# Kernel tuning notes

Hardware: AMD Instinct MI355X
Metric: run time of the kernel (lower is better)

The kernel has to match this reference:

```python
import jax, jax.numpy as jnp
import numpy as np

N = 20000      # nodes
E = 320000     # edges (avg degree 16)
IN, HID, OUT, H = 128, 32, 32, 8
NEG_SLOPE = 0.2


def _gat_conv(x, src, dst, W, al, ar, b):
    """One DGL-style GATConv. x: [N, F_in], W: [F_in, H*D], al/ar: [H, D], b: [H*D].
    Returns [N, H, D]."""
    n = x.shape[0]
    Hh, D = al.shape
    feat = (x @ W).reshape(n, Hh, D)                      # [N,H,D]
    el = jnp.sum(feat * al[None], axis=-1)                # [N,H]
    er = jnp.sum(feat * ar[None], axis=-1)                # [N,H]
    e = jax.nn.leaky_relu(el[src] + er[dst], NEG_SLOPE)   # [E,H]
    # edge softmax over incoming edges of each dst node (stable)
    emax = jax.ops.segment_max(e, dst, num_segments=n)    # [N,H]
    ee = jnp.exp(e - emax[dst])                           # [E,H]
    denom = jax.ops.segment_sum(ee, dst, num_segments=n)  # [N,H]
    alpha = ee / denom[dst]                               # [E,H]
    msg = feat[src] * alpha[:, :, None]                   # [E,H,D] gather+weight
    out = jax.ops.segment_sum(msg, dst, num_segments=n)   # [N,H,D] scatter-add
    return out + b.reshape(1, Hh, D)


def setup_inputs() -> dict:
    key = jax.random.key(0)
    ks = jax.random.split(key, 11)
    return {
        "x":   jax.random.normal(ks[0], (N, IN), dtype=jnp.float32),
        "src": jax.random.randint(ks[1], (E,), 0, N, dtype=jnp.int32),
        "dst": jax.random.randint(ks[2], (E,), 0, N, dtype=jnp.int32),
        "W1":  jax.random.normal(ks[3], (IN, H * HID), dtype=jnp.float32) * 0.1,
        "al1": jax.random.normal(ks[4], (H, HID), dtype=jnp.float32) * 0.1,
        "ar1": jax.random.normal(ks[5], (H, HID), dtype=jnp.float32) * 0.1,
        "b1":  jnp.zeros((H * HID,), dtype=jnp.float32),
        "W2":  jax.random.normal(ks[6], (HID, H * OUT), dtype=jnp.float32) * 0.1,
        "al2": jax.random.normal(ks[7], (H, OUT), dtype=jnp.float32) * 0.1,
        "ar2": jax.random.normal(ks[8], (H, OUT), dtype=jnp.float32) * 0.1,
        "b2":  jnp.zeros((H * OUT,), dtype=jnp.float32),
    }


def reference(x, src, dst, W1, al1, ar1, b1, W2, al2, ar2, b2):
    h = _gat_conv(x, src, dst, W1, al1, ar1, b1)          # [N,H,HID]
    h = jnp.mean(jax.nn.relu(h), axis=1)                  # [N,HID]
    h = _gat_conv(h, src, dst, W2, al2, ar2, b2)          # [N,H,OUT]
    return jnp.mean(h, axis=1)                            # [N,OUT]
```

## Files before the change

kernel.cpp:

```cpp
#include <hip/hip_runtime.h>
#include <hip/hip_bf16.h>

#define N_NODES 20000
#define N_EDGES 320000
#define F_IN    128
#define F_HID   32
#define NHEAD   8
#define FDIM    256
#define CAP     96

typedef __hip_bfloat16 bf16;
typedef __attribute__((ext_vector_type(8))) short short8;
typedef __attribute__((ext_vector_type(4))) float f32x4;

__device__ __forceinline__ unsigned short f2bf_rne(float f){
  unsigned u = __float_as_uint(f);
  unsigned r = u + 0x7FFFu + ((u >> 16) & 1u);
  return (unsigned short)(r >> 16);
}
__device__ __forceinline__ float bf2f(unsigned short s){
  return __uint_as_float((unsigned)s << 16);
}

#define FILLB  ((N_EDGES + 255) / 256)
#define SPLITB ((FDIM * (F_IN + F_HID)) / 256)
__global__ void prep_kernel(const int* __restrict__ src, const int* __restrict__ dst,
                            int* __restrict__ cnt, int* __restrict__ bucket,
                            const float* __restrict__ W1, const float* __restrict__ W2,
                            unsigned short* __restrict__ h1, unsigned short* __restrict__ l1,
                            unsigned short* __restrict__ h2, unsigned short* __restrict__ l2){
  const int b = blockIdx.x;
  if (b < FILLB){
    int i = b*256 + threadIdx.x;
    if (i < N_EDGES){
      int d = dst[i];
      int p = atomicAdd(&cnt[d], 1);
      if (p < CAP) bucket[(size_t)d*CAP + p] = src[i];
    }
  } else {
    int i = (b - FILLB)*256 + threadIdx.x;
    const int n1 = FDIM*F_IN;
    if (i < n1){
      int n = i / F_IN, k = i - n*F_IN;
      float v = W1[(size_t)k*FDIM + n];
      unsigned short hs = f2bf_rne(v);
      h1[i] = hs;
      l1[i] = f2bf_rne(v - bf2f(hs));
    } else {
      int j = i - n1;
      int n = j / F_HID, k = j - n*F_HID;
      float v = W2[(size_t)k*FDIM + n];
      unsigned short hs = f2bf_rne(v);
      h2[j] = hs;
      l2[j] = f2bf_rne(v - bf2f(hs));
    }
  }
}

template<int K, int XSPLIT>
__global__ __launch_bounds__(256) void gemm_mfma_kernel(
    const void* __restrict__ Xa, const void* __restrict__ Xb,
    const unsigned short* __restrict__ Wthi, const unsigned short* __restrict__ Wtlo,
    const float* __restrict__ al, const float* __restrict__ ar,
    unsigned short* __restrict__ feat, float* __restrict__ el, float* __restrict__ er)
{
  const int tid  = threadIdx.x;
  const int wv   = tid >> 6;
  const int lane = tid & 63;
  const int quad = lane >> 4;
  const int l16  = lane & 15;
  const int m0   = blockIdx.x * 16;
  constexpr int NC = K / 32;

  short8 Ah[NC], Al_[NC];
  if (XSPLIT){
    const float* xrow = (const float*)Xa + (size_t)(m0 + l16)*K;
    #pragma unroll
    for (int c = 0; c < NC; c++){
      float4 a0 = *(const float4*)(xrow + c*32 + quad*8);
      float4 a1 = *(const float4*)(xrow + c*32 + quad*8 + 4);
      const float vs[8] = {a0.x,a0.y,a0.z,a0.w,a1.x,a1.y,a1.z,a1.w};
      #pragma unroll
      for (int j = 0; j < 8; j++){
        unsigned short hs = f2bf_rne(vs[j]);
        Ah[c][j]  = (short)hs;
        Al_[c][j] = (short)f2bf_rne(vs[j] - bf2f(hs));
      }
    }
  } else {
    const size_t arow = (size_t)(m0 + l16) * K;
    #pragma unroll
    for (int c = 0; c < NC; c++){
      Ah[c]  = *(const short8*)((const unsigned short*)Xa + arow + c*32 + quad*8);
      Al_[c] = *(const short8*)((const unsigned short*)Xb + arow + c*32 + quad*8);
    }
  }

  float elp[8], erp[8];
  #pragma unroll
  for (int j = 0; j < 8; j++){ elp[j] = 0.f; erp[j] = 0.f; }

  #pragma unroll
  for (int t = 0; t < 4; t++){
    const int nc = wv*64 + t*16;
    const size_t brow = (size_t)(nc + l16) * K;
    f32x4 acc = {0.f, 0.f, 0.f, 0.f};
    #pragma unroll
    for (int c = 0; c < NC; c++){
      short8 Bh = *(const short8*)(Wthi + brow + c*32 + quad*8);
      short8 Bl = *(const short8*)(Wtlo + brow + c*32 + quad*8);
      acc = __builtin_amdgcn_mfma_f32_16x16x32_bf16(Ah[c],  Bh, acc, 0, 0, 0);
      acc = __builtin_amdgcn_mfma_f32_16x16x32_bf16(Ah[c],  Bl, acc, 0, 0, 0);
      acc = __builtin_amdgcn_mfma_f32_16x16x32_bf16(Al_[c], Bh, acc, 0, 0, 0);
    }
    const float alv = al[nc + l16];
    const float arv = ar[nc + l16];
    const int hl = t >> 1;
    #pragma unroll
    for (int r = 0; r < 4; r++){
      float v = acc[r];
      feat[(size_t)(m0 + quad*4 + r)*FDIM + nc + l16] = f2bf_rne(v);
      elp[r*2 + hl] = fmaf(v, alv, elp[r*2 + hl]);
      erp[r*2 + hl] = fmaf(v, arv, erp[r*2 + hl]);
    }
  }

  #pragma unroll
  for (int off = 1; off <= 8; off <<= 1){
    #pragma unroll
    for (int j = 0; j < 8; j++){
      elp[j] += __shfl_xor(elp[j], off);
      erp[j] += __shfl_xor(erp[j], off);
    }
  }
  __shared__ float el_lds[16][8], er_lds[16][8];
  if (l16 == 0){
    #pragma unroll
    for (int r = 0; r < 4; r++){
      #pragma unroll
      for (int hl = 0; hl < 2; hl++){
        el_lds[quad*4 + r][wv*2 + hl] = elp[r*2 + hl];
        er_lds[quad*4 + r][wv*2 + hl] = erp[r*2 + hl];
      }
    }
  }
  __syncthreads();
  if (tid < 128){
    int row = tid >> 3, h = tid & 7;
    el[(size_t)(m0 + row)*NHEAD + h] = el_lds[row][h];
    er[(size_t)(m0 + row)*NHEAD + h] = er_lds[row][h];
  }
}

template<int SPLIT_OUT>
__global__ __launch_bounds__(256) void edge_agg_kernel(
    const bf16* __restrict__ feat, const float* __restrict__ el,
    const float* __restrict__ er, const int* __restrict__ cnt,
    const int* __restrict__ bucket, const float* __restrict__ bias,
    float* __restrict__ outp,
    unsigned short* __restrict__ ohi, unsigned short* __restrict__ olo)
{
  const int tid  = threadIdx.x;
  const int wv   = tid >> 6;
  const int lane = tid & 63;
  const int n    = blockIdx.x*4 + wv;

  __shared__ float t_all[4][CAP*9];
  __shared__ int   s_all[4][CAP];
  __shared__ float sum_all[4][NHEAD];
  __shared__ float v_all[4][256];
  float* t_w = t_all[wv];
  int*   s_w = s_all[wv];

  int C = cnt[n];
  if (C > CAP) C = CAP;

  const float4* er4 = (const float4*)(er + (size_t)n*NHEAD);
  float4 era = er4[0], erb = er4[1];
  const float erv[8] = {era.x, era.y, era.z, era.w, erb.x, erb.y, erb.z, erb.w};

  for (int idx = lane; idx < C*2; idx += 64){
    const int e = idx >> 1, j = idx & 1;
    const int sidx = bucket[(size_t)n*CAP + e];
    if (j == 0) s_w[e] = sidx;
    float4 a = ((const float4*)(el + (size_t)sidx*NHEAD))[j];
    const float ev[4] = {a.x, a.y, a.z, a.w};
    #pragma unroll
    for (int hh = 0; hh < 4; hh++){
      float v = ev[hh] + erv[j*4 + hh];
      t_w[e*9 + j*4 + hh] = (v > 0.f) ? v : 0.2f*v;
    }
  }
  {
    const int h = lane >> 3, d = lane & 7;
    float lm = -INFINITY;
    for (int e = d; e < C; e += 8) lm = fmaxf(lm, t_w[e*9 + h]);
    #pragma unroll
    for (int off = 4; off >= 1; off >>= 1) lm = fmaxf(lm, __shfl_xor(lm, off));
    float ls = 0.f;
    for (int e = d; e < C; e += 8){
      float ex = __expf(t_w[e*9 + h] - lm);
      t_w[e*9 + h] = ex;
      ls += ex;
    }
    #pragma unroll
    for (int off = 4; off >= 1; off >>= 1) ls += __shfl_xor(ls, off);
    if (d == 0) sum_all[wv][h] = ls;
  }

  const int sub = lane >> 5;
  const int l   = lane & 31;
  const int hB  = l >> 2;
  const int coff = l << 3;
  float acc[8] = {0,0,0,0,0,0,0,0};
  int e = sub;
  float4 fv;
  if (e < C) fv = *(const float4*)(feat + (size_t)s_w[e]*FDIM + coff);
  while (e < C){
    const int en = e + 2;
    float4 fnext;
    if (en < C) fnext = *(const float4*)(feat + (size_t)s_w[en]*FDIM + coff);
    const float w = t_w[e*9 + hB];
    const unsigned* u = (const unsigned*)&fv;
    #pragma unroll
    for (int j = 0; j < 4; j++){
      float flo = __uint_as_float(u[j] << 16);
      float fhi = __uint_as_float(u[j] & 0xFFFF0000u);
      acc[2*j]   = fmaf(w, flo, acc[2*j]);
      acc[2*j+1] = fmaf(w, fhi, acc[2*j+1]);
    }
    fv = fnext;
    e = en;
  }
  #pragma unroll
  for (int j = 0; j < 8; j++) acc[j] += __shfl_xor(acc[j], 32);

  if (lane < 32){
    const float s = sum_all[wv][l >> 2];
    const float4* b4 = (const float4*)(bias + coff);
    float4 ba = b4[0], bb = b4[1];
    float bv[8] = {ba.x, ba.y, ba.z, ba.w, bb.x, bb.y, bb.z, bb.w};
    float v[8];
    #pragma unroll
    for (int j = 0; j < 8; j++){
      float val = (C > 0) ? (acc[j] / s) : 0.f;
      val += bv[j];
      if (SPLIT_OUT) val = fmaxf(val, 0.f);
      v[j] = val;
    }
    float4* v4 = (float4*)&v_all[wv][coff];
    v4[0] = make_float4(v[0], v[1], v[2], v[3]);
    v4[1] = make_float4(v[4], v[5], v[6], v[7]);
  }
  if (lane < 32){
    float sum = 0.f;
    #pragma unroll
    for (int hh = 0; hh < 8; hh++) sum += v_all[wv][hh*32 + lane];
    sum *= 0.125f;
    if (SPLIT_OUT){
      unsigned short hs = f2bf_rne(sum);
      ohi[(size_t)n*32 + lane] = hs;
      olo[(size_t)n*32 + lane] = f2bf_rne(sum - bf2f(hs));
    } else {
      outp[(size_t)n*32 + lane] = sum;
    }
  }
}

extern "C" void kernel_launch(void* const* d_in, const int* in_sizes, int n_in,
                              void* d_out, int out_size, void* d_ws, size_t ws_size,
                              hipStream_t stream)
{
  const float* x   = (const float*)d_in[0];
  const int*   src = (const int*)  d_in[1];
  const int*   dst = (const int*)  d_in[2];
  const float* W1  = (const float*)d_in[3];
  const float* al1 = (const float*)d_in[4];
  const float* ar1 = (const float*)d_in[5];
  const float* b1  = (const float*)d_in[6];
  const float* W2  = (const float*)d_in[7];
  const float* al2 = (const float*)d_in[8];
  const float* ar2 = (const float*)d_in[9];
  const float* b2  = (const float*)d_in[10];
  (void)in_sizes; (void)n_in; (void)out_size; (void)ws_size;

  size_t o = 0;
  char* base = (char*)d_ws;
  auto take = [&](size_t bytes) -> char* {
    char* p = base + o;
    o += (bytes + 255) & ~(size_t)255;
    return p;
  };
  unsigned short* feat  = (unsigned short*)take((size_t)N_NODES*FDIM*2);
  float* el     = (float*)take((size_t)N_NODES*NHEAD*4);
  float* er     = (float*)take((size_t)N_NODES*NHEAD*4);
  int*   cnt    = (int*)  take((size_t)N_NODES*4);
  int*   bucket = (int*)  take((size_t)N_NODES*CAP*4);
  unsigned short* Hhi  = (unsigned short*)take((size_t)N_NODES*F_HID*2);
  unsigned short* Hlo  = (unsigned short*)take((size_t)N_NODES*F_HID*2);
  unsigned short* W1th = (unsigned short*)take((size_t)FDIM*F_IN*2);
  unsigned short* W1tl = (unsigned short*)take((size_t)FDIM*F_IN*2);
  unsigned short* W2th = (unsigned short*)take((size_t)FDIM*F_HID*2);
  unsigned short* W2tl = (unsigned short*)take((size_t)FDIM*F_HID*2);

  hipMemsetAsync(cnt, 0, (size_t)N_NODES*4, stream);
  prep_kernel<<<FILLB + SPLITB, 256, 0, stream>>>(
      src, dst, cnt, bucket, W1, W2, W1th, W1tl, W2th, W2tl);

  gemm_mfma_kernel<F_IN, 1><<<N_NODES/16, 256, 0, stream>>>(
      x, nullptr, W1th, W1tl, al1, ar1, feat, el, er);
  edge_agg_kernel<1><<<N_NODES/4, 256, 0, stream>>>(
      (const bf16*)feat, el, er, cnt, bucket, b1, nullptr, Hhi, Hlo);

  gemm_mfma_kernel<F_HID, 0><<<N_NODES/16, 256, 0, stream>>>(
      Hhi, Hlo, W2th, W2tl, al2, ar2, feat, el, er);
  edge_agg_kernel<0><<<N_NODES/4, 256, 0, stream>>>(
      (const bf16*)feat, el, er, cnt, bucket, b2, (float*)d_out, nullptr, nullptr);
}
```

Measured before the change: 197.5 us.

## Fold layer-2 projection into aggregation: aggregate hidden features, then apply W2

Removes the layer-2 GEMM kernel. The attention logits el2/er2 are computed directly in the layer-1 aggregation from folded vectors W2·al2 and W2·ar2. The layer-2 aggregation now gathers 32-wide bf16 hidden rows instead of 256-wide projected features, and applies W2 per node after the weighted sum. This cuts gather traffic and one kernel launch. In exchange, each node does a small FP32 matvec, and the hidden features are stored as a single bf16 instead of a hi/lo split, which loses some precision.

```diff
diff --git a/kernel.cpp b/kernel.cpp
--- a/kernel.cpp
+++ b/kernel.cpp
@@ -23,12 +23,13 @@
 }
 
 #define FILLB  ((N_EDGES + 255) / 256)
-#define SPLITB ((FDIM * (F_IN + F_HID)) / 256)
 __global__ void prep_kernel(const int* __restrict__ src, const int* __restrict__ dst,
                             int* __restrict__ cnt, int* __restrict__ bucket,
                             const float* __restrict__ W1, const float* __restrict__ W2,
+                            const float* __restrict__ al2, const float* __restrict__ ar2,
                             unsigned short* __restrict__ h1, unsigned short* __restrict__ l1,
-                            unsigned short* __restrict__ h2, unsigned short* __restrict__ l2){
+                            float* __restrict__ W2t, float* __restrict__ q_lt,
+                            float* __restrict__ q_rt){
   const int b = blockIdx.x;
   if (b < FILLB){
     int i = b*256 + threadIdx.x;
@@ -37,29 +38,35 @@
       int p = atomicAdd(&cnt[d], 1);
       if (p < CAP) bucket[(size_t)d*CAP + p] = src[i];
     }
+  } else if (b < FILLB + 128){
+    int i = (b - FILLB)*256 + threadIdx.x;
+    int n = i >> 7, k = i & 127;
+    float v = W1[(size_t)k*FDIM + n];
+    unsigned short hs = f2bf_rne(v);
+    h1[i] = hs;
+    l1[i] = f2bf_rne(v - bf2f(hs));
+  } else if (b < FILLB + 160){
+    int i = (b - FILLB - 128)*256 + threadIdx.x;
+    int c = i >> 5, k = i & 31;
+    W2t[i] = W2[(size_t)k*FDIM + c];
   } else {
-    int i = (b - FILLB)*256 + threadIdx.x;
-    const int n1 = FDIM*F_IN;
-    if (i < n1){
-      int n = i / F_IN, k = i - n*F_IN;
-      float v = W1[(size_t)k*FDIM + n];
-      unsigned short hs = f2bf_rne(v);
-      h1[i] = hs;
-      l1[i] = f2bf_rne(v - bf2f(hs));
-    } else {
-      int j = i - n1;
-      int n = j / F_HID, k = j - n*F_HID;
-      float v = W2[(size_t)k*FDIM + n];
-      unsigned short hs = f2bf_rne(v);
-      h2[j] = hs;
-      l2[j] = f2bf_rne(v - bf2f(hs));
-    }
-  }
-}
-
-template<int K, int XSPLIT>
+    int t = threadIdx.x;
+    int k = t >> 3, hh = t & 7;
+    float sl = 0.f, sr = 0.f;
+    #pragma unroll
+    for (int d = 0; d < 32; d++){
+      float w = W2[(size_t)k*FDIM + hh*32 + d];
+      sl = fmaf(w, al2[hh*32 + d], sl);
+      sr = fmaf(w, ar2[hh*32 + d], sr);
+    }
+    q_lt[t] = sl;
+    q_rt[t] = sr;
+  }
+}
+
+template<int K>
 __global__ __launch_bounds__(256) void gemm_mfma_kernel(
-    const void* __restrict__ Xa, const void* __restrict__ Xb,
+    const float* __restrict__ X,
     const unsigned short* __restrict__ Wthi, const unsigned short* __restrict__ Wtlo,
     const float* __restrict__ al, const float* __restrict__ ar,
     unsigned short* __restrict__ feat, float* __restrict__ el, float* __restrict__ er)
@@ -73,8 +80,8 @@
   constexpr int NC = K / 32;
 
   short8 Ah[NC], Al_[NC];
-  if (XSPLIT){
-    const float* xrow = (const float*)Xa + (size_t)(m0 + l16)*K;
+  {
+    const float* xrow = X + (size_t)(m0 + l16)*K;
     #pragma unroll
     for (int c = 0; c < NC; c++){
       float4 a0 = *(const float4*)(xrow + c*32 + quad*8);
@@ -87,13 +94,6 @@
         Al_[c][j] = (short)f2bf_rne(vs[j] - bf2f(hs));
       }
     }
-  } else {
-    const size_t arow = (size_t)(m0 + l16) * K;
-    #pragma unroll
-    for (int c = 0; c < NC; c++){
-      Ah[c]  = *(const short8*)((const unsigned short*)Xa + arow + c*32 + quad*8);
-      Al_[c] = *(const short8*)((const unsigned short*)Xb + arow + c*32 + quad*8);
-    }
   }
 
   float elp[8], erp[8];
@@ -152,13 +152,13 @@
   }
 }
 
-template<int SPLIT_OUT>
-__global__ __launch_bounds__(256) void edge_agg_kernel(
+__global__ __launch_bounds__(256) void edge_agg_l1(
     const bf16* __restrict__ feat, const float* __restrict__ el,
     const float* __restrict__ er, const int* __restrict__ cnt,
     const int* __restrict__ bucket, const float* __restrict__ bias,
-    float* __restrict__ outp,
-    unsigned short* __restrict__ ohi, unsigned short* __restrict__ olo)
+    const float* __restrict__ q_lt, const float* __restrict__ q_rt,
+    unsigned short* __restrict__ h_out, float* __restrict__ el2,
+    float* __restrict__ er2)
 {
   const int tid  = threadIdx.x;
   const int wv   = tid >> 6;
@@ -245,7 +245,7 @@
     for (int j = 0; j < 8; j++){
       float val = (C > 0) ? (acc[j] / s) : 0.f;
       val += bv[j];
-      if (SPLIT_OUT) val = fmaxf(val, 0.f);
+      val = fmaxf(val, 0.f);
       v[j] = val;
     }
     float4* v4 = (float4*)&v_all[wv][coff];
@@ -253,17 +253,141 @@
     v4[1] = make_float4(v[4], v[5], v[6], v[7]);
   }
   if (lane < 32){
-    float sum = 0.f;
-    #pragma unroll
-    for (int hh = 0; hh < 8; hh++) sum += v_all[wv][hh*32 + lane];
-    sum *= 0.125f;
-    if (SPLIT_OUT){
-      unsigned short hs = f2bf_rne(sum);
-      ohi[(size_t)n*32 + lane] = hs;
-      olo[(size_t)n*32 + lane] = f2bf_rne(sum - bf2f(hs));
-    } else {
-      outp[(size_t)n*32 + lane] = sum;
-    }
+    float hsum = 0.f;
+    #pragma unroll
+    for (int hh = 0; hh < 8; hh++) hsum += v_all[wv][hh*32 + lane];
+    hsum *= 0.125f;
+    h_out[(size_t)n*32 + lane] = f2bf_rne(hsum);
+
+    float4 qa0 = ((const float4*)(q_lt + lane*8))[0];
+    float4 qa1 = ((const float4*)(q_lt + lane*8))[1];
+    float4 qb0 = ((const float4*)(q_rt + lane*8))[0];
+    float4 qb1 = ((const float4*)(q_rt + lane*8))[1];
+    float pl[8] = {hsum*qa0.x, hsum*qa0.y, hsum*qa0.z, hsum*qa0.w,
+                   hsum*qa1.x, hsum*qa1.y, hsum*qa1.z, hsum*qa1.w};
+    float pr[8] = {hsum*qb0.x, hsum*qb0.y, hsum*qb0.z, hsum*qb0.w,
+                   hsum*qb1.x, hsum*qb1.y, hsum*qb1.z, hsum*qb1.w};
+    #pragma unroll
+    for (int off = 1; off <= 16; off <<= 1){
+      #pragma unroll
+      for (int j = 0; j < 8; j++){
+        pl[j] += __shfl_xor(pl[j], off);
+        pr[j] += __shfl_xor(pr[j], off);
+      }
+    }
+    if (l == 0){
+      #pragma unroll
+      for (int j = 0; j < 8; j++){
+        el2[(size_t)n*NHEAD + j] = pl[j];
+        er2[(size_t)n*NHEAD + j] = pr[j];
+      }
+    }
+  }
+}
+
+__global__ __launch_bounds__(256) void edge_agg_l2(
+    const unsigned short* __restrict__ h_bf, const float* __restrict__ el2,
+    const float* __restrict__ er2, const int* __restrict__ cnt,
+    const int* __restrict__ bucket, const float* __restrict__ W2t,
+    const float* __restrict__ b2, float* __restrict__ outp)
+{
+  const int tid  = threadIdx.x;
+  const int wv   = tid >> 6;
+  const int lane = tid & 63;
+  const int n    = blockIdx.x*4 + wv;
+
+  __shared__ float t_all[4][CAP*9];
+  __shared__ int   s_all[4][CAP];
+  __shared__ float sum_all[4][NHEAD];
+  __shared__ float A_lds[4][8][33];
+  float* t_w = t_all[wv];
+  int*   s_w = s_all[wv];
+
+  int C = cnt[n];
+  if (C > CAP) C = CAP;
+
+  const float4* er4 = (const float4*)(er2 + (size_t)n*NHEAD);
+  float4 era = er4[0], erb = er4[1];
+  const float erv[8] = {era.x, era.y, era.z, era.w, erb.x, erb.y, erb.z, erb.w};
+
+  for (int idx = lane; idx < C*2; idx += 64){
+    const int e = idx >> 1, j = idx & 1;
+    const int sidx = bucket[(size_t)n*CAP + e];
+    if (j == 0) s_w[e] = sidx;
+    float4 a = ((const float4*)(el2 + (size_t)sidx*NHEAD))[j];
+    const float ev[4] = {a.x, a.y, a.z, a.w};
+    #pragma unroll
+    for (int hh = 0; hh < 4; hh++){
+      float v = ev[hh] + erv[j*4 + hh];
+      t_w[e*9 + j*4 + hh] = (v > 0.f) ? v : 0.2f*v;
+    }
+  }
+  {
+    const int h = lane >> 3, d = lane & 7;
+    float lm = -INFINITY;
+    for (int e = d; e < C; e += 8) lm = fmaxf(lm, t_w[e*9 + h]);
+    #pragma unroll
+    for (int off = 4; off >= 1; off >>= 1) lm = fmaxf(lm, __shfl_xor(lm, off));
+    float ls = 0.f;
+    for (int e = d; e < C; e += 8){
+      float ex = __expf(t_w[e*9 + h] - lm);
+      t_w[e*9 + h] = ex;
+      ls += ex;
+    }
+    #pragma unroll
+    for (int off = 4; off >= 1; off >>= 1) ls += __shfl_xor(ls, off);
+    if (d == 0) sum_all[wv][h] = ls;
+  }
+
+  const int h  = lane & 7;
+  const int dg = lane >> 3;
+  float A0=0.f, A1=0.f, A2=0.f, A3=0.f;
+  int e = 0;
+  ushort4 hv;
+  if (e < C) hv = *(const ushort4*)(h_bf + (size_t)s_w[e]*32 + dg*4);
+  while (e < C){
+    const int en = e + 1;
+    ushort4 hnext;
+    if (en < C) hnext = *(const ushort4*)(h_bf + (size_t)s_w[en]*32 + dg*4);
+    const float w = t_w[e*9 + h];
+    A0 = fmaf(w, bf2f(hv.x), A0);
+    A1 = fmaf(w, bf2f(hv.y), A1);
+    A2 = fmaf(w, bf2f(hv.z), A2);
+    A3 = fmaf(w, bf2f(hv.w), A3);
+    hv = hnext;
+    e = en;
+  }
+  {
+    const float s = sum_all[wv][h];
+    const float inv = (C > 0) ? (1.f / s) : 0.f;
+    A_lds[wv][h][dg*4 + 0] = A0 * inv;
+    A_lds[wv][h][dg*4 + 1] = A1 * inv;
+    A_lds[wv][h][dg*4 + 2] = A2 * inv;
+    A_lds[wv][h][dg*4 + 3] = A3 * inv;
+  }
+
+  const int d  = lane & 31;
+  const int hw = lane >> 5;
+  float o = 0.f;
+  #pragma unroll
+  for (int h4 = 0; h4 < 4; h4++){
+    const int hh = hw*4 + h4;
+    const float* wrow = W2t + (size_t)(hh*32 + d)*32;
+    #pragma unroll
+    for (int k4 = 0; k4 < 8; k4++){
+      float4 w4 = ((const float4*)wrow)[k4];
+      o = fmaf(w4.x, A_lds[wv][hh][k4*4 + 0], o);
+      o = fmaf(w4.y, A_lds[wv][hh][k4*4 + 1], o);
+      o = fmaf(w4.z, A_lds[wv][hh][k4*4 + 2], o);
+      o = fmaf(w4.w, A_lds[wv][hh][k4*4 + 3], o);
+    }
+  }
+  o += __shfl_xor(o, 32);
+  if (lane < 32){
+    float bm = 0.f;
+    #pragma unroll
+    for (int hh = 0; hh < 8; hh++) bm += b2[hh*32 + d];
+    outp[(size_t)n*32 + d] = (o + bm) * 0.125f;
   }
 }
 
@@ -292,28 +416,28 @@
     return p;
   };
   unsigned short* feat  = (unsigned short*)take((size_t)N_NODES*FDIM*2);
-  float* el     = (float*)take((size_t)N_NODES*NHEAD*4);
-  float* er     = (float*)take((size_t)N_NODES*NHEAD*4);
+  float* el1    = (float*)take((size_t)N_NODES*NHEAD*4);
+  float* er1    = (float*)take((size_t)N_NODES*NHEAD*4);
+  float* el2    = (float*)take((size_t)N_NODES*NHEAD*4);
+  float* er2    = (float*)take((size_t)N_NODES*NHEAD*4);
   int*   cnt    = (int*)  take((size_t)N_NODES*4);
   int*   bucket = (int*)  take((size_t)N_NODES*CAP*4);
-  unsigned short* Hhi  = (unsigned short*)take((size_t)N_NODES*F_HID*2);
-  unsigned short* Hlo  = (unsigned short*)take((size_t)N_NODES*F_HID*2);
+  unsigned short* hbf  = (unsigned short*)take((size_t)N_NODES*F_HID*2);
   unsigned short* W1th = (unsigned short*)take((size_t)FDIM*F_IN*2);
   unsigned short* W1tl = (unsigned short*)take((size_t)FDIM*F_IN*2);
-  unsigned short* W2th = (unsigned short*)take((size_t)FDIM*F_HID*2);
-  unsigned short* W2tl = (unsigned short*)take((size_t)FDIM*F_HID*2);
+  float* W2t    = (float*)take((size_t)FDIM*F_HID*4);
+  float* q_lt   = (float*)take((size_t)F_HID*NHEAD*4);
+  float* q_rt   = (float*)take((size_t)F_HID*NHEAD*4);
 
   hipMemsetAsync(cnt, 0, (size_t)N_NODES*4, stream);
-  prep_kernel<<<FILLB + SPLITB, 256, 0, stream>>>(
-      src, dst, cnt, bucket, W1, W2, W1th, W1tl, W2th, W2tl);
-
-  gemm_mfma_kernel<F_IN, 1><<<N_NODES/16, 256, 0, stream>>>(
-      x, nullptr, W1th, W1tl, al1, ar1, feat, el, er);
-  edge_agg_kernel<1><<<N_NODES/4, 256, 0, stream>>>(
-      (const bf16*)feat, el, er, cnt, bucket, b1, nullptr, Hhi, Hlo);
-
-  gemm_mfma_kernel<F_HID, 0><<<N_NODES/16, 256, 0, stream>>>(
-      Hhi, Hlo, W2th, W2tl, al2, ar2, feat, el, er);
-  edge_agg_kernel<0><<<N_NODES/4, 256, 0, stream>>>(
-      (const bf16*)feat, el, er, cnt, bucket, b2, (float*)d_out, nullptr, nullptr);
-}
+  prep_kernel<<<FILLB + 161, 256, 0, stream>>>(
+      src, dst, cnt, bucket, W1, W2, al2, ar2, W1th, W1tl, W2t, q_lt, q_rt);
+
+  gemm_mfma_kernel<F_IN><<<N_NODES/16, 256, 0, stream>>>(
+      x, W1th, W1tl, al1, ar1, feat, el1, er1);
+  edge_agg_l1<<<N_NODES/4, 256, 0, stream>>>(
+      (const bf16*)feat, el1, er1, cnt, bucket, b1, q_lt, q_rt, hbf, el2, er2);
+
+  edge_agg_l2<<<N_NODES/4, 256, 0, stream>>>(
+      hbf, el2, er2, cnt, bucket, W2t, b2, (float*)d_out);
+}
```

Result: slower. 250.8 us (+27.0%).
